# Kernel optimization log

Hardware: AMD Instinct MI355X
Metric: run time of the kernel (lower is better)

Reference implementation:

```python
import jax, jax.numpy as jnp
import numpy as np

N_NODES = 100000
N_EDGES = 3200000
IN_DIM = 64
HID_DIM = 128
OUT_DIM = 2


def setup_inputs() -> dict:
    key = jax.random.key(0)
    k1, k2, k3, k4, k5, k6 = jax.random.split(key, 6)
    x = jax.random.normal(k1, (N_NODES, IN_DIM), dtype=jnp.float32)
    edge_index = jax.random.randint(k2, (2, N_EDGES), 0, N_NODES, dtype=jnp.int64)
    W_gcn = jax.random.normal(k3, (IN_DIM, HID_DIM), dtype=jnp.float32) / np.sqrt(IN_DIM)
    b_gcn = jax.random.normal(k4, (HID_DIM,), dtype=jnp.float32) * 0.02
    W_lin = jax.random.normal(k5, (HID_DIM, OUT_DIM), dtype=jnp.float32) / np.sqrt(HID_DIM)
    b_lin = jax.random.normal(k6, (OUT_DIM,), dtype=jnp.float32) * 0.02
    return {"x": x, "edge_index": edge_index, "W_gcn": W_gcn, "b_gcn": b_gcn,
            "W_lin": W_lin, "b_lin": b_lin}


def reference(x, edge_index, W_gcn, b_gcn, W_lin, b_lin):
    # GCNConv (PyG semantics): add self-loops, symmetric deg^{-1/2} norm,
    # aggregate source->target, then relu, dropout(eval=identity), linear.
    N = x.shape[0]
    loop = jnp.arange(N, dtype=edge_index.dtype)
    src = jnp.concatenate([edge_index[0], loop])  # message sources
    dst = jnp.concatenate([edge_index[1], loop])  # message targets

    h = x @ W_gcn  # [N, HID] - transform before propagate (GCNConv order)

    ones = jnp.ones(dst.shape, dtype=h.dtype)
    deg = jax.ops.segment_sum(ones, dst, num_segments=N)  # in-degree incl. self-loop
    dinv = jnp.where(deg > 0, jax.lax.rsqrt(deg), 0.0)
    norm = dinv[src] * dinv[dst]  # [E+N]

    msg = h[src] * norm[:, None]                      # irregular gather
    agg = jax.ops.segment_sum(msg, dst, num_segments=N)  # irregular scatter-add
    agg = agg + b_gcn

    # relu -> dropout(p=0.5, eval mode => identity) -> linear head
    return jax.nn.relu(agg) @ W_lin + b_lin  # [N, OUT_DIM]
```

## Files before the change

### kernel.cpp

```cpp
#include <hip/hip_runtime.h>
#include <hip/hip_fp16.h>

#define N_NODES 100000
#define N_EDGES 3200000
#define IN_DIM 64
#define HID_DIM 128

#define RNODES 128
#define NRANGE 782
#define PCHUNK 256
#define PCHSZ (N_EDGES / PCHUNK)
#define TCAP 48
#define NLCAP 4608

#define TILE(c, r) ((size_t)(c) * NRANGE + (r))

__global__ __launch_bounds__(1024) void part_kernel(const int* __restrict__ src,
                                                    const int* __restrict__ dst,
                                                    int* __restrict__ tmp,
                                                    int* __restrict__ tcnt) {
    __shared__ int cur[NRANGE];
    const int c = blockIdx.x, tid = threadIdx.x;
    for (int i = tid; i < NRANGE; i += 1024) cur[i] = 0;
    __syncthreads();
    const int e0 = c * PCHSZ;
    int* tmpc = tmp + TILE(c, 0) * TCAP;
    int i = tid;
    for (; i + 1024 < PCHSZ; i += 2048) {
        const int d0 = dst[e0 + i];
        const int s0 = src[e0 + i];
        const int d1 = dst[e0 + i + 1024];
        const int s1 = src[e0 + i + 1024];
        const int r0 = d0 >> 7;
        const int p0 = atomicAdd(&cur[r0], 1);
        if (p0 < TCAP) tmpc[(size_t)r0 * TCAP + p0] = s0 | ((d0 & 127) << 17);
        const int r1 = d1 >> 7;
        const int p1 = atomicAdd(&cur[r1], 1);
        if (p1 < TCAP) tmpc[(size_t)r1 * TCAP + p1] = s1 | ((d1 & 127) << 17);
    }
    if (i < PCHSZ) {
        const int d = dst[e0 + i];
        const int s = src[e0 + i];
        const int r = d >> 7;
        const int pos = atomicAdd(&cur[r], 1);
        if (pos < TCAP) tmpc[(size_t)r * TCAP + pos] = s | ((d & 127) << 17);
    }
    __syncthreads();
    for (int j = tid; j < NRANGE; j += 1024)
        tcnt[c * NRANGE + j] = min(cur[j], TCAP);
}

__global__ __launch_bounds__(512) void degscale_kernel(const int* __restrict__ tmp,
                                                       const int* __restrict__ tcnt,
                                                       const float* __restrict__ x,
                                                       int* __restrict__ degn,
                                                       float* __restrict__ dinv,
                                                       __half* __restrict__ y) {
    __shared__ int   cnt[RNODES];
    __shared__ float dvs[RNODES];
    const int r = blockIdx.x, tid = threadIdx.x;
    if (tid < RNODES) cnt[tid] = 0;
    __syncthreads();
    {
        const int c = tid & 255, half = tid >> 8;
        const int n = tcnt[c * NRANGE + r];
        const int* t = tmp + TILE(c, r) * TCAP;
        for (int i = half; i < n; i += 2) atomicAdd(&cnt[t[i] >> 17], 1);
    }
    __syncthreads();
    if (tid < RNODES) {
        const int node = r * RNODES + tid;
        const int dg = cnt[tid];
        degn[node] = dg;
        const float dv = rsqrtf((float)dg + 1.0f);
        dvs[tid] = dv;
        if (node < N_NODES) dinv[node] = dv;
    }
    __syncthreads();
    for (int i = tid; i < RNODES * 16; i += 512) {
        const int nl = i >> 4, q = i & 15;
        const int node = r * RNODES + nl;
        if (node < N_NODES) {
            const float4 v = ((const float4*)x)[(size_t)node * 16 + q];
            const float dv = dvs[nl];
            __half2 h0 = __floats2half2_rn(v.x * dv, v.y * dv);
            __half2 h1 = __floats2half2_rn(v.z * dv, v.w * dv);
            uint2 pk;
            pk.x = *(unsigned int*)&h0;
            pk.y = *(unsigned int*)&h1;
            ((uint2*)y)[(size_t)node * 16 + q] = pk;
        }
    }
}

__global__ __launch_bounds__(1024) void aggb_kernel(const int* __restrict__ tmp,
                                                    const int* __restrict__ tcnt,
                                                    const int* __restrict__ degn,
                                                    const __half* __restrict__ y,
                                                    __half* __restrict__ agg) {
    __shared__ int nodelist[NLCAP];
    __shared__ int sc[RNODES];
    __shared__ int start[RNODES];
    __shared__ int cur[RNODES];
    const int r = blockIdx.x, tid = threadIdx.x;

    int mydeg = 0;
    if (tid < RNODES) {
        mydeg = degn[r * RNODES + tid];
        sc[tid] = mydeg;
    }
    __syncthreads();
    #pragma unroll
    for (int off = 1; off < RNODES; off <<= 1) {
        int v = 0;
        if (tid < RNODES && tid >= off) v = sc[tid - off];
        __syncthreads();
        if (tid < RNODES) sc[tid] += v;
        __syncthreads();
    }
    if (tid < RNODES) {
        start[tid] = sc[tid] - mydeg;
        cur[tid]   = sc[tid] - mydeg;
    }
    __syncthreads();

    {
        const int c = tid & 255, ph = tid >> 8;
        const int n = tcnt[c * NRANGE + r];
        const int* t = tmp + TILE(c, r) * TCAP;
        for (int i = ph; i < n; i += 4) {
            const int pk = t[i];
            const int slot = atomicAdd(&cur[pk >> 17], 1);
            if (slot < NLCAP) nodelist[slot] = pk & 0x1FFFF;
        }
    }
    __syncthreads();

    const int g = tid >> 3, lane = tid & 7;
    const uint4* y16 = (const uint4*)y;
    const int node = r * RNODES + g;
    if (node < N_NODES) {
        float accf[8];
        {
            const uint4 pk = y16[(size_t)node * 8 + lane];
            const __half2* h = (const __half2*)&pk;
            #pragma unroll
            for (int q = 0; q < 4; ++q) {
                const float2 f = __half22float2(h[q]);
                accf[2*q] = f.x; accf[2*q+1] = f.y;
            }
        }
        const int beg = start[g], end = sc[g];
        int j = beg;
        for (; j + 4 <= end; j += 4) {
            const int s0 = nodelist[j];
            const int s1 = nodelist[j + 1];
            const int s2 = nodelist[j + 2];
            const int s3 = nodelist[j + 3];
            const uint4 p0 = y16[(size_t)s0 * 8 + lane];
            const uint4 p1 = y16[(size_t)s1 * 8 + lane];
            const uint4 p2 = y16[(size_t)s2 * 8 + lane];
            const uint4 p3 = y16[(size_t)s3 * 8 + lane];
            const __half2* h0 = (const __half2*)&p0;
            const __half2* h1 = (const __half2*)&p1;
            const __half2* h2 = (const __half2*)&p2;
            const __half2* h3 = (const __half2*)&p3;
            #pragma unroll
            for (int q = 0; q < 4; ++q) {
                float2 f0 = __half22float2(h0[q]);
                float2 f1 = __half22float2(h1[q]);
                float2 f2 = __half22float2(h2[q]);
                float2 f3 = __half22float2(h3[q]);
                accf[2*q]   += (f0.x + f1.x) + (f2.x + f3.x);
                accf[2*q+1] += (f0.y + f1.y) + (f2.y + f3.y);
            }
        }
        for (; j < end; ++j) {
            const int s = nodelist[j];
            const uint4 pk = y16[(size_t)s * 8 + lane];
            const __half2* h = (const __half2*)&pk;
            #pragma unroll
            for (int q = 0; q < 4; ++q) {
                const float2 f = __half22float2(h[q]);
                accf[2*q] += f.x; accf[2*q+1] += f.y;
            }
        }
        uint4 o;
        __half2* oh = (__half2*)&o;
        #pragma unroll
        for (int q = 0; q < 4; ++q)
            oh[q] = __floats2half2_rn(accf[2*q], accf[2*q+1]);
        ((uint4*)agg)[(size_t)node * 8 + lane] = o;
    }
}

#define H_NPB 32
__global__ __launch_bounds__(256) void head_kernel(const __half* __restrict__ agg,
                                                   const float* __restrict__ dinv,
                                                   const float* __restrict__ W,
                                                   const float* __restrict__ b_gcn,
                                                   const float* __restrict__ W_lin,
                                                   const float* __restrict__ b_lin,
                                                   float* __restrict__ out) {
    __shared__ float4 Ws[IN_DIM * HID_DIM / 4];
    __shared__ float  as[H_NPB * IN_DIM];
    const int tid = threadIdx.x;

    const float4* W4 = (const float4*)W;
    #pragma unroll
    for (int i = tid; i < IN_DIM * HID_DIM / 4; i += 256) Ws[i] = W4[i];

    const int node0 = blockIdx.x * H_NPB;
    {
        const uint4 a4 = ((const uint4*)(agg + (size_t)node0 * IN_DIM))[tid];
        const __half2* h = (const __half2*)&a4;
        #pragma unroll
        for (int q = 0; q < 4; ++q) {
            const float2 f = __half22float2(h[q]);
            as[tid * 8 + 2*q]     = f.x;
            as[tid * 8 + 2*q + 1] = f.y;
        }
    }
    __syncthreads();

    const int jq = tid & 31;
    const int ng = tid >> 5;
    const float* arow = as + ng * 4 * IN_DIM;

    float4 a0 = {0,0,0,0}, a1 = {0,0,0,0}, a2 = {0,0,0,0}, a3 = {0,0,0,0};
    for (int k = 0; k < IN_DIM; ++k) {
        const float4 wv = Ws[k * 32 + jq];
        const float v0 = arow[k];
        const float v1 = arow[IN_DIM + k];
        const float v2 = arow[2 * IN_DIM + k];
        const float v3 = arow[3 * IN_DIM + k];
        a0.x += v0*wv.x; a0.y += v0*wv.y; a0.z += v0*wv.z; a0.w += v0*wv.w;
        a1.x += v1*wv.x; a1.y += v1*wv.y; a1.z += v1*wv.z; a1.w += v1*wv.w;
        a2.x += v2*wv.x; a2.y += v2*wv.y; a2.z += v2*wv.z; a2.w += v2*wv.w;
        a3.x += v3*wv.x; a3.y += v3*wv.y; a3.z += v3*wv.z; a3.w += v3*wv.w;
    }

    const float4 bg = ((const float4*)b_gcn)[jq];
    const int c0 = jq * 4;
    const float w00 = W_lin[(c0+0)*2], w01 = W_lin[(c0+0)*2+1];
    const float w10 = W_lin[(c0+1)*2], w11 = W_lin[(c0+1)*2+1];
    const float w20 = W_lin[(c0+2)*2], w21 = W_lin[(c0+2)*2+1];
    const float w30 = W_lin[(c0+3)*2], w31 = W_lin[(c0+3)*2+1];
    const float bl0 = b_lin[0], bl1 = b_lin[1];

    float4 am[4] = {a0, a1, a2, a3};
    #pragma unroll
    for (int m = 0; m < 4; ++m) {
        const int node = node0 + ng * 4 + m;
        const float dv = dinv[node];
        float4 v;
        v.x = fmaxf(am[m].x * dv + bg.x, 0.f);
        v.y = fmaxf(am[m].y * dv + bg.y, 0.f);
        v.z = fmaxf(am[m].z * dv + bg.z, 0.f);
        v.w = fmaxf(am[m].w * dv + bg.w, 0.f);
        float o0 = v.x*w00 + v.y*w10 + v.z*w20 + v.w*w30;
        float o1 = v.x*w01 + v.y*w11 + v.z*w21 + v.w*w31;
        #pragma unroll
        for (int off = 16; off > 0; off >>= 1) {
            o0 += __shfl_down(o0, off, 32);
            o1 += __shfl_down(o1, off, 32);
        }
        if (jq == 0) {
            out[(size_t)node * 2 + 0] = o0 + bl0;
            out[(size_t)node * 2 + 1] = o1 + bl1;
        }
    }
}

extern "C" void kernel_launch(void* const* d_in, const int* in_sizes, int n_in,
                              void* d_out, int out_size, void* d_ws, size_t ws_size,
                              hipStream_t stream) {
    const float* x     = (const float*)d_in[0];
    const int*   ei    = (const int*)  d_in[1];
    const float* W_gcn = (const float*)d_in[2];
    const float* b_gcn = (const float*)d_in[3];
    const float* W_lin = (const float*)d_in[4];
    const float* b_lin = (const float*)d_in[5];
    float* out = (float*)d_out;

    int*    tmp  = (int*)d_ws;
    int*    tcnt = tmp + (size_t)NRANGE * PCHUNK * TCAP;
    int*    degn = tcnt + NRANGE * PCHUNK;
    float*  dinv = (float*)(degn + NRANGE * RNODES);
    __half* y    = (__half*)(dinv + N_NODES);
    __half* agg  = y + (size_t)N_NODES * IN_DIM;

    const int* src = ei;
    const int* dst = ei + N_EDGES;

    part_kernel<<<PCHUNK, 1024, 0, stream>>>(src, dst, tmp, tcnt);
    degscale_kernel<<<NRANGE, 512, 0, stream>>>(tmp, tcnt, x, degn, dinv, y);
    aggb_kernel<<<NRANGE, 1024, 0, stream>>>(tmp, tcnt, degn, y, agg);
    head_kernel<<<N_NODES / H_NPB, 256, 0, stream>>>(agg, dinv, W_gcn, b_gcn, W_lin, b_lin, out);
}
```

Before: 227.3 us.

## Fuse neighbor aggregation with GCN transform and linear head kernel

The head computation (64x128 matmul, bias, ReLU, 128x2 linear) now runs inside the aggregation kernel. The aggregated fp16 rows stay in shared memory instead of going to a global buffer that a separate kernel reads back. This removes one launch, the global write and read of the aggregate, and the repeated per-block W loads of the old small head blocks. In exchange the aggregation blocks use more shared memory (the W tile plus the row tile), which may lower occupancy, and they do extra compute after the gather phase. Out-of-range nodes in the last block are guarded.

```diff
diff --git a/kernel.cpp b/kernel.cpp
--- a/kernel.cpp
+++ b/kernel.cpp
@@ -93,16 +93,27 @@
     }
 }
 
-__global__ __launch_bounds__(1024) void aggb_kernel(const int* __restrict__ tmp,
+__global__ __launch_bounds__(1024) void aggh_kernel(const int* __restrict__ tmp,
                                                     const int* __restrict__ tcnt,
                                                     const int* __restrict__ degn,
                                                     const __half* __restrict__ y,
-                                                    __half* __restrict__ agg) {
-    __shared__ int nodelist[NLCAP];
-    __shared__ int sc[RNODES];
-    __shared__ int start[RNODES];
-    __shared__ int cur[RNODES];
+                                                    const float* __restrict__ dinv,
+                                                    const float* __restrict__ W,
+                                                    const float* __restrict__ b_gcn,
+                                                    const float* __restrict__ W_lin,
+                                                    const float* __restrict__ b_lin,
+                                                    float* __restrict__ out) {
+    __shared__ int    nodelist[NLCAP];
+    __shared__ int    sc[RNODES];
+    __shared__ int    start[RNODES];
+    __shared__ int    cur[RNODES];
+    __shared__ __half as[RNODES * IN_DIM];
+    __shared__ float4 Ws[IN_DIM * HID_DIM / 4];
     const int r = blockIdx.x, tid = threadIdx.x;
+
+    const float4* W4 = (const float4*)W;
+    Ws[tid] = W4[tid];
+    Ws[tid + 1024] = W4[tid + 1024];
 
     int mydeg = 0;
     if (tid < RNODES) {
@@ -138,11 +149,11 @@
 
     const int g = tid >> 3, lane = tid & 7;
     const uint4* y16 = (const uint4*)y;
-    const int node = r * RNODES + g;
-    if (node < N_NODES) {
+    const int gnode = r * RNODES + g;
+    if (gnode < N_NODES) {
         float accf[8];
         {
-            const uint4 pk = y16[(size_t)node * 8 + lane];
+            const uint4 pk = y16[(size_t)gnode * 8 + lane];
             const __half2* h = (const __half2*)&pk;
             #pragma unroll
             for (int q = 0; q < 4; ++q) {
@@ -190,50 +201,24 @@
         #pragma unroll
         for (int q = 0; q < 4; ++q)
             oh[q] = __floats2half2_rn(accf[2*q], accf[2*q+1]);
-        ((uint4*)agg)[(size_t)node * 8 + lane] = o;
-    }
-}
-
-#define H_NPB 32
-__global__ __launch_bounds__(256) void head_kernel(const __half* __restrict__ agg,
-                                                   const float* __restrict__ dinv,
-                                                   const float* __restrict__ W,
-                                                   const float* __restrict__ b_gcn,
-                                                   const float* __restrict__ W_lin,
-                                                   const float* __restrict__ b_lin,
-                                                   float* __restrict__ out) {
-    __shared__ float4 Ws[IN_DIM * HID_DIM / 4];
-    __shared__ float  as[H_NPB * IN_DIM];
-    const int tid = threadIdx.x;
-
-    const float4* W4 = (const float4*)W;
-    #pragma unroll
-    for (int i = tid; i < IN_DIM * HID_DIM / 4; i += 256) Ws[i] = W4[i];
-
-    const int node0 = blockIdx.x * H_NPB;
-    {
-        const uint4 a4 = ((const uint4*)(agg + (size_t)node0 * IN_DIM))[tid];
-        const __half2* h = (const __half2*)&a4;
-        #pragma unroll
-        for (int q = 0; q < 4; ++q) {
-            const float2 f = __half22float2(h[q]);
-            as[tid * 8 + 2*q]     = f.x;
-            as[tid * 8 + 2*q + 1] = f.y;
-        }
+        ((uint4*)as)[g * 8 + lane] = o;
+    } else {
+        const uint4 z = {0, 0, 0, 0};
+        ((uint4*)as)[g * 8 + lane] = z;
     }
     __syncthreads();
 
     const int jq = tid & 31;
     const int ng = tid >> 5;
-    const float* arow = as + ng * 4 * IN_DIM;
+    const __half* arow = as + ng * 4 * IN_DIM;
 
     float4 a0 = {0,0,0,0}, a1 = {0,0,0,0}, a2 = {0,0,0,0}, a3 = {0,0,0,0};
     for (int k = 0; k < IN_DIM; ++k) {
         const float4 wv = Ws[k * 32 + jq];
-        const float v0 = arow[k];
-        const float v1 = arow[IN_DIM + k];
-        const float v2 = arow[2 * IN_DIM + k];
-        const float v3 = arow[3 * IN_DIM + k];
+        const float v0 = __half2float(arow[k]);
+        const float v1 = __half2float(arow[IN_DIM + k]);
+        const float v2 = __half2float(arow[2 * IN_DIM + k]);
+        const float v3 = __half2float(arow[3 * IN_DIM + k]);
         a0.x += v0*wv.x; a0.y += v0*wv.y; a0.z += v0*wv.z; a0.w += v0*wv.w;
         a1.x += v1*wv.x; a1.y += v1*wv.y; a1.z += v1*wv.z; a1.w += v1*wv.w;
         a2.x += v2*wv.x; a2.y += v2*wv.y; a2.z += v2*wv.z; a2.w += v2*wv.w;
@@ -251,8 +236,8 @@
     float4 am[4] = {a0, a1, a2, a3};
     #pragma unroll
     for (int m = 0; m < 4; ++m) {
-        const int node = node0 + ng * 4 + m;
-        const float dv = dinv[node];
+        const int node = r * RNODES + ng * 4 + m;
+        const float dv = (node < N_NODES) ? dinv[node] : 0.f;
         float4 v;
         v.x = fmaxf(am[m].x * dv + bg.x, 0.f);
         v.y = fmaxf(am[m].y * dv + bg.y, 0.f);
@@ -265,7 +250,7 @@
             o0 += __shfl_down(o0, off, 32);
             o1 += __shfl_down(o1, off, 32);
         }
-        if (jq == 0) {
+        if (jq == 0 && node < N_NODES) {
             out[(size_t)node * 2 + 0] = o0 + bl0;
             out[(size_t)node * 2 + 1] = o1 + bl1;
         }
@@ -288,13 +273,12 @@
     int*    degn = tcnt + NRANGE * PCHUNK;
     float*  dinv = (float*)(degn + NRANGE * RNODES);
     __half* y    = (__half*)(dinv + N_NODES);
-    __half* agg  = y + (size_t)N_NODES * IN_DIM;
 
     const int* src = ei;
     const int* dst = ei + N_EDGES;
 
     part_kernel<<<PCHUNK, 1024, 0, stream>>>(src, dst, tmp, tcnt);
     degscale_kernel<<<NRANGE, 512, 0, stream>>>(tmp, tcnt, x, degn, dinv, y);
-    aggb_kernel<<<NRANGE, 1024, 0, stream>>>(tmp, tcnt, degn, y, agg);
-    head_kernel<<<N_NODES / H_NPB, 256, 0, stream>>>(agg, dinv, W_gcn, b_gcn, W_lin, b_lin, out);
-}
+    aggh_kernel<<<NRANGE, 1024, 0, stream>>>(tmp, tcnt, degn, y, dinv,
+                                             W_gcn, b_gcn, W_lin, b_lin, out);
+}
```

New measurement: 232.9 us. 2.5% more time.
